# Optimization experiments

Hardware: AMD Instinct MI355X
Metric: run time of the kernel (lower is better)

## Reference

```python
import jax, jax.numpy as jnp
import numpy as np

ODE_UNFOLDS = 6
MOTOR_SIZE = 3
EPS = 1e-8

def _conv(x, w, b, stride):
    y = jax.lax.conv_general_dilated(x, w, (stride, stride), 'VALID',
                                     dimension_numbers=('NCHW', 'OIHW', 'NCHW'))
    return jax.nn.relu(y + b[None, :, None, None])

def _conv_head(x, w1, b1, w2, b2, w3, b3, w4, b4, w5, b5, fc_w, fc_b):
    # x: [B, T, 3, 66, 200] -> features [B, T, 128]
    B, T = x.shape[0], x.shape[1]
    h = x.reshape(B * T, *x.shape[2:])
    h = _conv(h, w1, b1, 2)  # [BT,24,31,98]
    h = _conv(h, w2, b2, 2)  # [BT,36,14,47]
    h = _conv(h, w3, b3, 2)  # [BT,48,5,22]
    h = _conv(h, w4, b4, 1)  # [BT,64,3,20]
    h = _conv(h, w5, b5, 1)  # [BT,64,1,18]
    h = h.reshape(B * T, -1)
    h = jax.nn.relu(h @ fc_w + fc_b)
    return h.reshape(B, T, -1)

def _ltc_step(inputs, v, s_mu, s_sigma, s_w, s_erev, mu, sigma, w, erev, gleak, vleak, cm):
    # inputs: [B,S], v: [B,N]
    # sensory synapse activations (constant over the ODE unfolds)
    s_act = s_w * jax.nn.sigmoid((inputs[:, :, None] - s_mu) * s_sigma)  # [B,S,N]
    w_num_s = jnp.sum(s_act * s_erev, axis=1)  # [B,N]
    w_den_s = jnp.sum(s_act, axis=1)           # [B,N]
    cm_t = cm * ODE_UNFOLDS  # cm / (elapsed=1 / ode_unfolds)
    for _ in range(ODE_UNFOLDS):
        w_act = w * jax.nn.sigmoid((v[:, :, None] - mu) * sigma)  # [B,N,N]
        w_num = jnp.sum(w_act * erev, axis=1) + w_num_s
        w_den = jnp.sum(w_act, axis=1) + w_den_s
        v = (cm_t * v + gleak * vleak + w_num) / (cm_t + gleak + w_den + EPS)
    return v[:, :MOTOR_SIZE], v

def reference(x, w1, b1, w2, b2, w3, b3, w4, b4, w5, b5, fc_w, fc_b,
              s_mu, s_sigma, s_w, s_erev, mu, sigma, w, erev, gleak, vleak, cm):
    y = _conv_head(x, w1, b1, w2, b2, w3, b3, w4, b4, w5, b5, fc_w, fc_b)  # [B,T,128]
    B, T, _ = y.shape
    N = mu.shape[0]
    v0 = jnp.zeros((B, N), dtype=y.dtype)

    def step(v, inp):
        out, v = _ltc_step(inp, v, s_mu, s_sigma, s_w, s_erev, mu, sigma, w, erev, gleak, vleak, cm)
        return v, out

    _, outs = jax.lax.scan(step, v0, jnp.swapaxes(y, 0, 1))  # outs: [T,B,3]
    return jnp.swapaxes(outs, 0, 1)  # [B,T,3]

def setup_inputs() -> dict:
    key = jax.random.key(0)
    ks = jax.random.split(key, 24)
    d = {}
    d['x'] = jax.random.normal(ks[0], (32, 16, 3, 66, 200), jnp.float32)
    shapes = [((24, 3, 5, 5), (24,)), ((36, 24, 5, 5), (36,)), ((48, 36, 5, 5), (48,)),
              ((64, 48, 3, 3), (64,)), ((64, 64, 3, 3), (64,))]
    for i, (ws, bs) in enumerate(shapes):
        d[f'w{i+1}'] = jax.random.normal(ks[1 + i], ws, jnp.float32) * 0.05
        d[f'b{i+1}'] = jnp.zeros(bs, jnp.float32)
    d['fc_w'] = jax.random.normal(ks[6], (1152, 128), jnp.float32) * 0.05
    d['fc_b'] = jnp.zeros((128,), jnp.float32)
    S, N = 128, 64
    d['s_mu'] = jax.random.normal(ks[7], (S, N), jnp.float32) * 0.3 + 0.3
    d['s_sigma'] = jax.random.uniform(ks[8], (S, N), jnp.float32, 3.0, 8.0)
    d['s_w'] = jax.random.uniform(ks[9], (S, N), jnp.float32, 0.001, 1.0)
    d['s_erev'] = jnp.sign(jax.random.normal(ks[10], (S, N), jnp.float32))
    d['mu'] = jax.random.normal(ks[11], (N, N), jnp.float32) * 0.3 + 0.3
    d['sigma'] = jax.random.uniform(ks[12], (N, N), jnp.float32, 3.0, 8.0)
    d['w'] = jax.random.uniform(ks[13], (N, N), jnp.float32, 0.001, 1.0)
    d['erev'] = jnp.sign(jax.random.normal(ks[14], (N, N), jnp.float32))
    d['gleak'] = jax.random.uniform(ks[15], (N,), jnp.float32, 0.001, 1.0)
    d['vleak'] = jax.random.uniform(ks[16], (N,), jnp.float32, -0.2, 0.2)
    d['cm'] = jax.random.uniform(ks[17], (N,), jnp.float32, 0.4, 0.6)
    return d
```

## Files before the change

kernel.cpp:

```cpp
#include <hip/hip_runtime.h>
#include <hip/hip_bf16.h>


typedef _Float16 f16;
typedef _Float16 f16x8 __attribute__((ext_vector_type(8)));
typedef _Float16 f16x4 __attribute__((ext_vector_type(4)));
typedef float    f32x4 __attribute__((ext_vector_type(4)));
typedef unsigned int u32;

static __device__ __forceinline__ float sigmoidf_fast(float x) {
    return __builtin_amdgcn_rcpf(1.0f + __expf(-x));
}


__global__ __launch_bounds__(256)
void wpack1_kernel(const float* __restrict__ w1, f16* __restrict__ Wpk1)
{
    int idx = blockIdx.x * 256 + threadIdx.x;
    if (idx >= 32 * 136) return;
    int co = idx / 136;
    int kk = idx % 136;
    float v = 0.0f;
    if (co < 24 && kk < 120) {
        int p = kk >> 3, jj = kk & 7;
        int kh = p / 3, kwp = p % 3;
        int kws = jj >> 2, ci = jj & 3;
        int kw = 2 * kwp + kws;
        if (kw < 5 && ci < 3)
            v = w1[(((size_t)co * 3 + ci) * 5 + kh) * 5 + kw];
    }
    Wpk1[idx] = (f16)v;
}

__global__ __launch_bounds__(512)
void conv1_mfma(const float* __restrict__ x, const f16* __restrict__ Wpk1,
                const float* __restrict__ b1, f16* __restrict__ h1T)
{
    __shared__ __align__(16) f16 img[52800];
    __shared__ __align__(16) f16 Wl[4352];

    int m    = blockIdx.x;
    int tid  = threadIdx.x;
    int lane = tid & 63;
    int wv   = tid >> 6;
    int col  = lane & 15;
    int row4 = lane >> 4;

    for (int u = tid; u < 544; u += 512)
        *(uint4*)((char*)Wl + (size_t)u * 16) =
            *(const uint4*)((const char*)Wpk1 + (size_t)u * 16);

    const float* xb = x + (size_t)m * 39600;
    for (int u = tid; u < 13200; u += 512) {
        float a = xb[u], b = xb[13200 + u], c = xb[26400 + u];
        f16x4 pk = { (f16)a, (f16)b, (f16)c, (f16)0.0f };
        *(f16x4*)(&img[(size_t)u * 4]) = pk;
    }
    __syncthreads();

    f16x8 af[2][4];
    #pragma unroll
    for (int Mt = 0; Mt < 2; ++Mt)
        #pragma unroll
        for (int t = 0; t < 4; ++t)
            af[Mt][t] = *(const f16x8*)((const char*)Wl +
                           (Mt * 16 + col) * 272 + t * 64 + row4 * 16);

    int rowB[4], kwpv[4];
    #pragma unroll
    for (int t = 0; t < 4; ++t) {
        int p = 4 * t + row4; if (p > 14) p = 14;
        rowB[t] = (p / 3) * 1600;
        kwpv[t] = (p % 3) * 16;
    }

    float bvv[2][4];
    #pragma unroll
    for (int Mt = 0; Mt < 2; ++Mt)
        #pragma unroll
        for (int i = 0; i < 4; ++i) {
            int co = Mt * 16 + row4 * 4 + i;
            bvv[Mt][i] = (co < 24) ? b1[co] : 0.0f;
        }

    const char* ic = (const char*)img;
    for (int it = 0; it < 24; ++it) {
        int s = wv + it * 8;
        if (s * 16 >= 3038) continue;
        int px = s * 16 + col;
        bool pv = (px < 3038);
        int pc = pv ? px : 3037;
        int ho = pc / 98;
        int wo = pc - ho * 98;
        int base = ho * 3200 + wo * 16;

        f32x4 a0 = {0.f,0.f,0.f,0.f}, a1 = {0.f,0.f,0.f,0.f};
        #pragma unroll
        for (int t = 0; t < 4; ++t) {
            f16x8 xf = *(const f16x8*)(ic + base + rowB[t] + kwpv[t]);
            a0 = __builtin_amdgcn_mfma_f32_16x16x32_f16(af[0][t], xf, a0, 0, 0, 0);
            a1 = __builtin_amdgcn_mfma_f32_16x16x32_f16(af[1][t], xf, a1, 0, 0, 0);
        }

        if (pv) {
            size_t rowbase = ((size_t)m * 31 + ho) * 296;
            int par = (wo & 1) * 49, wh = wo >> 1;
            int j0 = (row4 & 1) * 4;
            {
                int c8 = row4 >> 1;
                f16x4 pk = { (f16)fmaxf(a0[0] + bvv[0][0], 0.0f),
                             (f16)fmaxf(a0[1] + bvv[0][1], 0.0f),
                             (f16)fmaxf(a0[2] + bvv[0][2], 0.0f),
                             (f16)fmaxf(a0[3] + bvv[0][3], 0.0f) };
                int sl = c8 * 98 + par + wh;
                *(f16x4*)(h1T + (rowbase + sl) * 8 + j0) = pk;
            }
            if (row4 < 2) {
                f16x4 pk = { (f16)fmaxf(a1[0] + bvv[1][0], 0.0f),
                             (f16)fmaxf(a1[1] + bvv[1][1], 0.0f),
                             (f16)fmaxf(a1[2] + bvv[1][2], 0.0f),
                             (f16)fmaxf(a1[3] + bvv[1][3], 0.0f) };
                int sl = 2 * 98 + par + wh;
                *(f16x4*)(h1T + (rowbase + sl) * 8 + j0) = pk;
            }
        }
    }
}

__global__ __launch_bounds__(256)
void wpack_kernel(const float* __restrict__ w2, f16* __restrict__ Wpk)
{
    int idx = blockIdx.x * 256 + threadIdx.x;
    if (idx >= 48 * 616) return;
    int co = idx / 616;
    int kk = idx % 616;
    float v = 0.0f;
    if (kk < 608 && co < 36) {
        int c = kk >> 3, j = kk & 7;
        if (c < 75) {
            int pq = c / 3, c8 = c - 3 * pq;
            int kh = pq / 5, kw = pq - 5 * kh;
            int ci = c8 * 8 + j;
            v = w2[(((size_t)co * 24 + ci) * 5 + kh) * 5 + kw];
        }
    }
    Wpk[idx] = (f16)v;
}

__global__ __launch_bounds__(256)
void wpack3_kernel(const float* __restrict__ w3, f16* __restrict__ Wpk3)
{
    int idx = blockIdx.x * 256 + threadIdx.x;
    if (idx >= 48 * 1032) return;
    int co = idx / 1032;
    int kk = idx % 1032;
    float v = 0.0f;
    if (kk < 1024) {
        int c = kk >> 3, j = kk & 7;
        int pq = c / 5, c8 = c - 5 * pq;
        if (pq < 25) {
            int kh = pq / 5, kw = pq - 5 * kh;
            int ci = c8 * 8 + j;
            if (ci < 36)
                v = w3[(((size_t)co * 36 + ci) * 5 + kh) * 5 + kw];
        }
    }
    Wpk3[idx] = (f16)v;
}

__global__ __launch_bounds__(384, 3)
void conv2_mfma(const f16* __restrict__ h1T, const f16* __restrict__ Wpk,
                const float* __restrict__ b2, f16* __restrict__ h2f)
{
    __shared__ __align__(16) f16 tl[2][7 * 2368];
    __shared__ u32 lutS[76];

    int m    = blockIdx.x;
    int tid  = threadIdx.x;
    int lane = tid & 63;
    int wv   = tid >> 6;
    int ct   = wv >> 1;
    int sh   = wv & 1;
    int row4 = lane >> 4;
    int col  = lane & 15;

    if (tid < 76) {
        int c = tid; u32 v = 0;
        if (c < 75) {
            int pq = c / 3, c8 = c - 3 * pq;
            int kh = pq / 5, kw = pq - 5 * kh;
            u32 ofs = (u32)(c8 * 98 + (kw & 1) * 49 + (kw >> 1));
            v = ((u32)(kh * 4736) << 8) | ofs;
        }
        lutS[c] = v;
    }

    f16x8 af[19];
    {
        const char* wb = (const char*)Wpk + (size_t)(ct * 16 + col) * 1232 + row4 * 16;
        #pragma unroll
        for (int t = 0; t < 19; ++t)
            af[t] = *(const f16x8*)(wb + t * 64);
    }

    int wo16[3], rpoff[3], valid[3], wov[3];
    #pragma unroll
    for (int si = 0; si < 3; ++si) {
        int s  = 3 * sh + si;
        int px = 16 * s + col;
        int rp = (px >= 48) ? 1 : 0;
        int wo = px - 48 * rp;
        valid[si] = (wo < 47);
        int wog = wo < 47 ? wo : 46;
        wo16[si]  = wog * 16;
        wov[si]   = wo;
        rpoff[si] = rp * 9472;
    }
    float bv[4];
    #pragma unroll
    for (int i = 0; i < 4; ++i) {
        int co = ct * 16 + row4 * 4 + i;
        bv[i] = (co < 36) ? b2[co] : 0.0f;
    }
    int c8o  = ct * 2 + (row4 >> 1);
    int hsel = (row4 & 1) * 4;

    uint4 stg[6];
    const f16* imgbase = h1T + (size_t)m * 31 * 2368;

    {
        const char* g = (const char*)(imgbase);
        #pragma unroll
        for (int i = 0; i < 6; ++i) {
            int u = tid + i * 384;
            if (u < 2072) *(uint4*)((char*)tl[0] + (size_t)u * 16) =
                              *(const uint4*)(g + (size_t)u * 16);
        }
    }
    __syncthreads();

    for (int p = 0; p < 7; ++p) {
        int cur = p & 1;
        if (p < 6) {
            const char* g = (const char*)(imgbase + (size_t)(4 * (p + 1)) * 2368);
            #pragma unroll
            for (int i = 0; i < 6; ++i) {
                int u = tid + i * 384;
                if (u < 2072) stg[i] = *(const uint4*)(g + (size_t)u * 16);
            }
        }

        const char* tb = (const char*)tl[cur];
        f32x4 acc0 = {0.f,0.f,0.f,0.f}, acc1 = {0.f,0.f,0.f,0.f}, acc2 = {0.f,0.f,0.f,0.f};
        #pragma unroll
        for (int t = 0; t < 19; ++t) {
            u32 lv   = lutS[4 * t + row4];
            int rowb = (int)(lv >> 8);
            int boff = (int)(lv & 255) << 4;
            f16x8 a = af[t];
            {
                f16x8 xf = *(const f16x8*)(tb + rpoff[0] + rowb + boff + wo16[0]);
                acc0 = __builtin_amdgcn_mfma_f32_16x16x32_f16(a, xf, acc0, 0, 0, 0);
            }
            {
                f16x8 xf = *(const f16x8*)(tb + rpoff[1] + rowb + boff + wo16[1]);
                acc1 = __builtin_amdgcn_mfma_f32_16x16x32_f16(a, xf, acc1, 0, 0, 0);
            }
            {
                f16x8 xf = *(const f16x8*)(tb + rpoff[2] + rowb + boff + wo16[2]);
                acc2 = __builtin_amdgcn_mfma_f32_16x16x32_f16(a, xf, acc2, 0, 0, 0);
            }
        }

        #pragma unroll
        for (int si = 0; si < 3; ++si) {
            f32x4 a = (si == 0) ? acc0 : (si == 1) ? acc1 : acc2;
            int s  = 3 * sh + si;
            int px = 16 * s + col;
            int rp = (px >= 48) ? 1 : 0;
            int wo = px - 48 * rp;
            int ho = 2 * p + rp;
            if (valid[si] && c8o < 5) {
                f16x4 pk;
                #pragma unroll
                for (int i = 0; i < 4; ++i) pk[i] = (f16)fmaxf(a[i] + bv[i], 0.0f);
                int sl = c8o * 47 + (wo & 1) * 24 + (wo >> 1);
                *(f16x4*)(h2f + ((size_t)m * 3374 + (size_t)ho * 241 + sl) * 8 + hsel) = pk;
            }
        }

        if (p < 6) {
            #pragma unroll
            for (int i = 0; i < 6; ++i) {
                int u = tid + i * 384;
                if (u < 2072) *(uint4*)((char*)tl[cur ^ 1] + (size_t)u * 16) = stg[i];
            }
        }
        __syncthreads();
    }
}

__global__ __launch_bounds__(384)
void conv3_mfma(const f16* __restrict__ h2f, const f16* __restrict__ Wpk3,
                const float* __restrict__ b3, float* __restrict__ h3)
{
    __shared__ __align__(16) f16 Wl[48 * 1032];
    __shared__ __align__(16) f16 img[3374 * 8];
    __shared__ u32 lut[128];

    int m    = blockIdx.x;
    int tid  = threadIdx.x;
    int lane = tid & 63;
    int wv   = tid >> 6;
    int ct   = wv >> 1;
    int sh   = wv & 1;
    int row4 = lane >> 4;
    int col  = lane & 15;

    if (tid < 128) {
        int c  = tid;
        int pq = c / 5, c8 = c - 5 * pq;
        int kh = pq / 5, kw = pq - 5 * kh;
        lut[c] = ((u32)(kh * 3856) << 8) |
                 (u32)(c8 * 47 + (kw & 1) * 24 + (kw >> 1));
    }
    for (int u = tid; u < 6192; u += 384)
        *(uint4*)((char*)Wl + (size_t)u * 16) =
            *(const uint4*)((const char*)Wpk3 + (size_t)u * 16);
    {
        const char* g = (const char*)(h2f + (size_t)m * 3374 * 8);
        for (int u = tid; u < 3374; u += 384)
            *(uint4*)((char*)img + (size_t)u * 16) = *(const uint4*)(g + (size_t)u * 16);
    }
    __syncthreads();

    int rb[4], wo16[4], valid[4], hov[4], wov[4];
    int nsi = 4 - sh;
    #pragma unroll
    for (int si = 0; si < 4; ++si) {
        int s  = 4 * sh + si;
        int px = 16 * s + col;
        valid[si] = (si < nsi) && (px < 110);
        int pc = px < 110 ? px : 109;
        int ho = pc / 22, wo = pc - 22 * ho;
        rb[si]   = ho * 7712;
        wo16[si] = wo * 16;
        hov[si]  = ho; wov[si] = wo;
    }

    float bv[4];
    #pragma unroll
    for (int i = 0; i < 4; ++i) bv[i] = b3[ct * 16 + row4 * 4 + i];

    int Abase = (ct * 16 + col) * 2064 + row4 * 16;
    const char* Wc = (const char*)Wl;
    const char* ic = (const char*)img;

    f32x4 a0 = {0.f,0.f,0.f,0.f}, a1 = {0.f,0.f,0.f,0.f};
    f32x4 a2 = {0.f,0.f,0.f,0.f}, a3 = {0.f,0.f,0.f,0.f};
    #pragma unroll 8
    for (int t = 0; t < 32; ++t) {
        u32 lv     = lut[4 * t + row4];
        int rowoff = (int)(lv >> 8);
        int boff   = (int)(lv & 255) << 4;
        f16x8 af = *(const f16x8*)(Wc + Abase + 64 * t);
        {
            f16x8 xf = *(const f16x8*)(ic + rb[0] + rowoff + boff + wo16[0]);
            a0 = __builtin_amdgcn_mfma_f32_16x16x32_f16(af, xf, a0, 0, 0, 0);
        }
        {
            f16x8 xf = *(const f16x8*)(ic + rb[1] + rowoff + boff + wo16[1]);
            a1 = __builtin_amdgcn_mfma_f32_16x16x32_f16(af, xf, a1, 0, 0, 0);
        }
        {
            f16x8 xf = *(const f16x8*)(ic + rb[2] + rowoff + boff + wo16[2]);
            a2 = __builtin_amdgcn_mfma_f32_16x16x32_f16(af, xf, a2, 0, 0, 0);
        }
        {
            f16x8 xf = *(const f16x8*)(ic + rb[3] + rowoff + boff + wo16[3]);
            a3 = __builtin_amdgcn_mfma_f32_16x16x32_f16(af, xf, a3, 0, 0, 0);
        }
    }

    int co0 = ct * 16 + row4 * 4;
    #pragma unroll
    for (int si = 0; si < 4; ++si) {
        if (!valid[si]) continue;
        f32x4 a = (si == 0) ? a0 : (si == 1) ? a1 : (si == 2) ? a2 : a3;
        float* op = h3 + (((size_t)m * 48 + co0) * 5 + hov[si]) * 22 + wov[si];
        #pragma unroll
        for (int i = 0; i < 4; ++i)
            op[(size_t)i * 110] = fmaxf(a[i] + bv[i], 0.0f);
    }
}

template<int CIN, int KH, int KW, int STRIDE, int CO_T, int WO_T>
__global__ __launch_bounds__(256)
void conv_tile_kernel(const float* __restrict__ in, const float* __restrict__ wt,
                      const float* __restrict__ bias, float* __restrict__ out,
                      int Cout, int Hin, int Win, int Hout, int Wout,
                      int n_cg, int n_wg, int M)
{
    constexpr int LOAD_W = (WO_T - 1) * STRIDE + KW;

    int bx = blockIdx.x;
    int cg = bx % n_cg;
    int gid = (bx / n_cg) * blockDim.x + threadIdx.x;
    int wg = gid % n_wg;
    int t  = gid / n_wg;
    int ho = t % Hout;
    int m  = t / Hout;
    if (m >= M) return;

    int wo0 = wg * WO_T;
    int co0 = cg * CO_T;

    const float* ip = in + ((size_t)(m * CIN) * Hin + (size_t)ho * STRIDE) * Win
                         + (size_t)wo0 * STRIDE;
    const float* wp = wt + (size_t)co0 * (CIN * KH * KW);

    float acc[CO_T][WO_T];
    #pragma unroll
    for (int c = 0; c < CO_T; ++c) {
        float b = bias[co0 + c];
        #pragma unroll
        for (int q = 0; q < WO_T; ++q) acc[c][q] = b;
    }

    #pragma unroll 1
    for (int ci = 0; ci < CIN; ++ci) {
        #pragma unroll
        for (int kh = 0; kh < KH; ++kh) {
            const float* row = ip + ((size_t)ci * Hin + kh) * Win;
            float xv[LOAD_W];
            #pragma unroll
            for (int l = 0; l < LOAD_W; ++l) xv[l] = row[l];
            const float* wrow = wp + (ci * KH + kh) * KW;
            #pragma unroll
            for (int c = 0; c < CO_T; ++c) {
                #pragma unroll
                for (int kw = 0; kw < KW; ++kw) {
                    float wv = wrow[c * (CIN * KH * KW) + kw];
                    #pragma unroll
                    for (int q = 0; q < WO_T; ++q)
                        acc[c][q] = fmaf(xv[q * STRIDE + kw], wv, acc[c][q]);
                }
            }
        }
    }

    #pragma unroll
    for (int c = 0; c < CO_T; ++c) {
        float* op = out + (((size_t)m * Cout + co0 + c) * Hout + ho) * Wout + wo0;
        #pragma unroll
        for (int q = 0; q < WO_T; ++q) {
            if (wo0 + q < Wout) op[q] = fmaxf(acc[c][q], 0.0f);
        }
    }
}

__global__ __launch_bounds__(256)
void fc_relu_kernel(const float* __restrict__ h, const float* __restrict__ w,
                    const float* __restrict__ b, float* __restrict__ out)
{
    __shared__ float hs[1152];
    __shared__ float part[8][32][4];
    int f   = blockIdx.x;
    int tid = threadIdx.x;
    int ks  = tid >> 5;
    int j4  = tid & 31;
    for (int k = tid; k < 1152; k += 256) hs[k] = h[(size_t)f * 1152 + k];
    __syncthreads();
    const float4* w4 = (const float4*)w;
    float4 acc = {0.f, 0.f, 0.f, 0.f};
    int k0 = ks * 144;
    #pragma unroll 4
    for (int kk = 0; kk < 144; ++kk) {
        int k = k0 + kk;
        float4 wv = w4[(size_t)k * 32 + j4];
        float hb = hs[k];
        acc.x = fmaf(wv.x, hb, acc.x);
        acc.y = fmaf(wv.y, hb, acc.y);
        acc.z = fmaf(wv.z, hb, acc.z);
        acc.w = fmaf(wv.w, hb, acc.w);
    }
    *(float4*)&part[ks][j4][0] = acc;
    __syncthreads();
    if (tid < 128) {
        int j = tid, jq = j >> 2, r = j & 3;
        float s = b[j];
        #pragma unroll
        for (int q = 0; q < 8; ++q) s += part[q][jq][r];
        out[(size_t)f * 128 + j] = fmaxf(s, 0.0f);
    }
}

__global__ __launch_bounds__(64)
void sensory_kernel(const float* __restrict__ feat,
                    const float* __restrict__ s_mu,
                    const float* __restrict__ s_sigma,
                    const float* __restrict__ s_w,
                    const float* __restrict__ s_erev,
                    float* __restrict__ wnum, float* __restrict__ wden)
{
    __shared__ float y[128];
    int bt = blockIdx.x;
    int n  = threadIdx.x;
    for (int s = n; s < 128; s += 64) y[s] = feat[bt * 128 + s];
    __syncthreads();
    float num = 0.0f, den = 0.0f;
    for (int s = 0; s < 128; ++s) {
        int o = s * 64 + n;
        float a = s_w[o] * sigmoidf_fast((y[s] - s_mu[o]) * s_sigma[o]);
        num = fmaf(a, s_erev[o], num);
        den += a;
    }
    wnum[bt * 64 + n] = num;
    wden[bt * 64 + n] = den;
}

__global__ __launch_bounds__(512)
void ltc_wave_kernel(const float* __restrict__ wnum_s,
                     const float* __restrict__ wden_s,
                     const float* __restrict__ mu, const float* __restrict__ sigma,
                     const float* __restrict__ w, const float* __restrict__ erev,
                     const float* __restrict__ gleak, const float* __restrict__ vleak,
                     const float* __restrict__ cm, float* __restrict__ out, int T)
{
    __shared__ float2 pnd[2][8][64];

    int b    = blockIdx.x;
    int tid  = threadIdx.x;
    int lane = tid & 63;
    int p    = tid >> 6;

    float musig[8], nsg[8], wv[8], wev[8];
    #pragma unroll
    for (int ii = 0; ii < 8; ++ii) {
        int o = (8 * p + ii) * 64 + lane;
        float sg = sigma[o];
        musig[ii] = mu[o] * sg;
        nsg[ii]   = -sg;
        float wl  = w[o];
        wv[ii]    = wl;
        wev[ii]   = wl * erev[o];
    }
    float gl   = gleak[lane];
    float glvl = gl * vleak[lane];
    float cmt  = cm[lane] * 6.0f;
    float v    = 0.0f;
    int   buf  = 0;

    for (int t = 0; t < T; ++t) {
        float ns = wnum_s[(b * T + t) * 64 + lane];
        float ds = wden_s[(b * T + t) * 64 + lane];
        #pragma unroll 1
        for (int u = 0; u < 6; ++u) {
            float num = 0.0f, den = 0.0f;
            #pragma unroll
            for (int ii = 0; ii < 8; ++ii) {
                float vi  = __shfl(v, 8 * p + ii);
                float arg = fmaf(vi, nsg[ii], musig[ii]);
                float e   = __expf(arg);
                float s   = __builtin_amdgcn_rcpf(1.0f + e);
                den = fmaf(wv[ii], s, den);
                num = fmaf(wev[ii], s, num);
            }
            pnd[buf][p][lane] = make_float2(num, den);
            __syncthreads();
            float wn = ns, wd = ds;
            #pragma unroll
            for (int q = 0; q < 8; ++q) {
                float2 pq = pnd[buf][q][lane];
                wn += pq.x; wd += pq.y;
            }
            v = (fmaf(cmt, v, glvl) + wn) *
                __builtin_amdgcn_rcpf(cmt + gl + wd + 1e-8f);
            buf ^= 1;
        }
        if (tid < 3) out[(b * T + t) * 3 + tid] = v;
    }
}

extern "C" void kernel_launch(void* const* d_in, const int* in_sizes, int n_in,
                              void* d_out, int out_size, void* d_ws, size_t ws_size,
                              hipStream_t stream)
{
    (void)in_sizes; (void)n_in; (void)out_size; (void)ws_size;

    const float* x    = (const float*)d_in[0];
    const float* w1   = (const float*)d_in[1];
    const float* b1   = (const float*)d_in[2];
    const float* w2   = (const float*)d_in[3];
    const float* b2   = (const float*)d_in[4];
    const float* w3   = (const float*)d_in[5];
    const float* b3   = (const float*)d_in[6];
    const float* w4   = (const float*)d_in[7];
    const float* b4   = (const float*)d_in[8];
    const float* w5   = (const float*)d_in[9];
    const float* b5   = (const float*)d_in[10];
    const float* fcw  = (const float*)d_in[11];
    const float* fcb  = (const float*)d_in[12];
    const float* smu  = (const float*)d_in[13];
    const float* ssig = (const float*)d_in[14];
    const float* sw   = (const float*)d_in[15];
    const float* serv = (const float*)d_in[16];
    const float* mu   = (const float*)d_in[17];
    const float* sig  = (const float*)d_in[18];
    const float* ww   = (const float*)d_in[19];
    const float* erev = (const float*)d_in[20];
    const float* gl   = (const float*)d_in[21];
    const float* vl   = (const float*)d_in[22];
    const float* cm   = (const float*)d_in[23];
    float* out = (float*)d_out;

    const int BT = 512;

    char* wsB = (char*)d_ws;
    size_t off = 0;
    f16*   h1T  = (f16*)(wsB + off); off += (size_t)512 * 31 * 2368 * 2;
    f16*   Wpk  = (f16*)(wsB + off); off += 65536;
    f16*   h2f  = (f16*)(wsB + off); off += (size_t)512 * 3374 * 16;
    f16*   Wpk3 = (f16*)(wsB + off); off += 48 * 1032 * 2;
    f16*   Wpk1 = (f16*)(wsB + off); off += 32 * 136 * 2;
    float* h3   = (float*)(wsB + off); off += (size_t)512 * 48 * 5 * 22 * 4;
    float* h4   = (float*)(wsB + off); off += (size_t)512 * 64 * 3 * 20 * 4;
    float* h5   = (float*)(wsB + off); off += (size_t)512 * 64 * 18 * 4;
    float* feat = (float*)(wsB + off); off += (size_t)BT * 128 * 4;
    float* wnum = (float*)(wsB + off); off += (size_t)BT * 64 * 4;
    float* wden = (float*)(wsB + off); off += (size_t)BT * 64 * 4;

    wpack1_kernel<<<(32 * 136 + 255) / 256, 256, 0, stream>>>(w1, Wpk1);
    wpack_kernel<<<(48 * 616 + 255) / 256, 256, 0, stream>>>(w2, Wpk);
    wpack3_kernel<<<(48 * 1032 + 255) / 256, 256, 0, stream>>>(w3, Wpk3);

    conv1_mfma<<<512, 512, 0, stream>>>(x, Wpk1, b1, h1T);
    conv2_mfma<<<512, 384, 0, stream>>>(h1T, Wpk, b2, h2f);
    conv3_mfma<<<512, 384, 0, stream>>>(h2f, Wpk3, b3, h3);

    {
        int n_cg = 16, n_wg = 5;
        int sp_threads = BT * 3 * n_wg;
        int grid = (sp_threads + 255) / 256 * n_cg;
        conv_tile_kernel<48, 3, 3, 1, 4, 4><<<grid, 256, 0, stream>>>(
            h3, w4, b4, h4, 64, 5, 22, 3, 20, n_cg, n_wg, BT);
    }
    {
        int n_cg = 16, n_wg = 6;
        int sp_threads = BT * 1 * n_wg;
        int grid = (sp_threads + 255) / 256 * n_cg;
        conv_tile_kernel<64, 3, 3, 1, 4, 3><<<grid, 256, 0, stream>>>(
            h4, w5, b5, h5, 64, 3, 20, 1, 18, n_cg, n_wg, BT);
    }
    fc_relu_kernel<<<512, 256, 0, stream>>>(h5, fcw, fcb, feat);
    sensory_kernel<<<BT, 64, 0, stream>>>(feat, smu, ssig, sw, serv, wnum, wden);
    ltc_wave_kernel<<<32, 512, 0, stream>>>(wnum, wden, mu, sig, ww, erev,
                                            gl, vl, cm, out, 16);
}
```

Baseline: 286.8 us.

## Load whole conv2 input image into LDS and tile pixels linearly

conv2 previously streamed seven-row slabs through a double-buffered LDS tile, with a barrier per slab and padding lanes wasted on each 48-wide row pair. The new version copies the full 31-row input image (about 147 KB) into shared memory once and then walks 658 output pixels in flat 16-pixel tiles, removing the per-slab barriers and the padding waste. The much larger LDS footprint drops occupancy to roughly one block per CU, and the load is no longer overlapped with compute.

```diff
diff --git a/kernel.cpp b/kernel.cpp
--- a/kernel.cpp
+++ b/kernel.cpp
@@ -168,11 +168,11 @@
     Wpk3[idx] = (f16)v;
 }
 
-__global__ __launch_bounds__(384, 3)
+__global__ __launch_bounds__(384)
 void conv2_mfma(const f16* __restrict__ h1T, const f16* __restrict__ Wpk,
                 const float* __restrict__ b2, f16* __restrict__ h2f)
 {
-    __shared__ __align__(16) f16 tl[2][7 * 2368];
+    __shared__ __align__(16) f16 img[73408];
     __shared__ u32 lutS[76];
 
     int m    = blockIdx.x;
@@ -203,19 +203,12 @@
             af[t] = *(const f16x8*)(wb + t * 64);
     }
 
-    int wo16[3], rpoff[3], valid[3], wov[3];
-    #pragma unroll
-    for (int si = 0; si < 3; ++si) {
-        int s  = 3 * sh + si;
-        int px = 16 * s + col;
-        int rp = (px >= 48) ? 1 : 0;
-        int wo = px - 48 * rp;
-        valid[si] = (wo < 47);
-        int wog = wo < 47 ? wo : 46;
-        wo16[si]  = wog * 16;
-        wov[si]   = wo;
-        rpoff[si] = rp * 9472;
-    }
+    {
+        const char* g = (const char*)(h1T + (size_t)m * 73408);
+        for (int u = tid; u < 9176; u += 384)
+            *(uint4*)((char*)img + (size_t)u * 16) = *(const uint4*)(g + (size_t)u * 16);
+    }
+
     float bv[4];
     #pragma unroll
     for (int i = 0; i < 4; ++i) {
@@ -225,32 +218,23 @@
     int c8o  = ct * 2 + (row4 >> 1);
     int hsel = (row4 & 1) * 4;
 
-    uint4 stg[6];
-    const f16* imgbase = h1T + (size_t)m * 31 * 2368;
-
-    {
-        const char* g = (const char*)(imgbase);
-        #pragma unroll
-        for (int i = 0; i < 6; ++i) {
-            int u = tid + i * 384;
-            if (u < 2072) *(uint4*)((char*)tl[0] + (size_t)u * 16) =
-                              *(const uint4*)(g + (size_t)u * 16);
-        }
-    }
     __syncthreads();
 
-    for (int p = 0; p < 7; ++p) {
-        int cur = p & 1;
-        if (p < 6) {
-            const char* g = (const char*)(imgbase + (size_t)(4 * (p + 1)) * 2368);
-            #pragma unroll
-            for (int i = 0; i < 6; ++i) {
-                int u = tid + i * 384;
-                if (u < 2072) stg[i] = *(const uint4*)(g + (size_t)u * 16);
-            }
-        }
-
-        const char* tb = (const char*)tl[cur];
+    const char* ic = (const char*)img;
+    for (int it = 0; it < 7; ++it) {
+        int rbase[3], valid[3], hov[3], wov[3];
+        #pragma unroll
+        for (int si = 0; si < 3; ++si) {
+            int tile = sh * 21 + it * 3 + si;
+            int px   = tile * 16 + col;
+            valid[si] = (px < 658);
+            int pc = valid[si] ? px : 657;
+            int ho = pc / 47;
+            int wo = pc - 47 * ho;
+            rbase[si] = ho * 9472 + wo * 16;
+            hov[si] = ho; wov[si] = wo;
+        }
+
         f32x4 acc0 = {0.f,0.f,0.f,0.f}, acc1 = {0.f,0.f,0.f,0.f}, acc2 = {0.f,0.f,0.f,0.f};
         #pragma unroll
         for (int t = 0; t < 19; ++t) {
@@ -259,15 +243,15 @@
             int boff = (int)(lv & 255) << 4;
             f16x8 a = af[t];
             {
-                f16x8 xf = *(const f16x8*)(tb + rpoff[0] + rowb + boff + wo16[0]);
+                f16x8 xf = *(const f16x8*)(ic + rbase[0] + rowb + boff);
                 acc0 = __builtin_amdgcn_mfma_f32_16x16x32_f16(a, xf, acc0, 0, 0, 0);
             }
             {
-                f16x8 xf = *(const f16x8*)(tb + rpoff[1] + rowb + boff + wo16[1]);
+                f16x8 xf = *(const f16x8*)(ic + rbase[1] + rowb + boff);
                 acc1 = __builtin_amdgcn_mfma_f32_16x16x32_f16(a, xf, acc1, 0, 0, 0);
             }
             {
-                f16x8 xf = *(const f16x8*)(tb + rpoff[2] + rowb + boff + wo16[2]);
+                f16x8 xf = *(const f16x8*)(ic + rbase[2] + rowb + boff);
                 acc2 = __builtin_amdgcn_mfma_f32_16x16x32_f16(a, xf, acc2, 0, 0, 0);
             }
         }
@@ -275,12 +259,8 @@
         #pragma unroll
         for (int si = 0; si < 3; ++si) {
             f32x4 a = (si == 0) ? acc0 : (si == 1) ? acc1 : acc2;
-            int s  = 3 * sh + si;
-            int px = 16 * s + col;
-            int rp = (px >= 48) ? 1 : 0;
-            int wo = px - 48 * rp;
-            int ho = 2 * p + rp;
             if (valid[si] && c8o < 5) {
+                int wo = wov[si], ho = hov[si];
                 f16x4 pk;
                 #pragma unroll
                 for (int i = 0; i < 4; ++i) pk[i] = (f16)fmaxf(a[i] + bv[i], 0.0f);
@@ -288,15 +268,6 @@
                 *(f16x4*)(h2f + ((size_t)m * 3374 + (size_t)ho * 241 + sl) * 8 + hsel) = pk;
             }
         }
-
-        if (p < 6) {
-            #pragma unroll
-            for (int i = 0; i < 6; ++i) {
-                int u = tid + i * 384;
-                if (u < 2072) *(uint4*)((char*)tl[cur ^ 1] + (size_t)u * 16) = stg[i];
-            }
-        }
-        __syncthreads();
     }
 }
 
```

Result: faster. 268.5 us (-6.4%).
